# Optimization experiments

Hardware: AMD Instinct MI355X
Metric: run time of the kernel (lower is better)

The kernel has to match this reference:

```python
import jax, jax.numpy as jnp
import numpy as np

B, S, D, H, F = 2, 2048, 1024, 16, 4096
HD = D // H
EPS = 1e-5
NEG = -1e9


def _layernorm(x, g, b):
    mu = jnp.mean(x, axis=-1, keepdims=True)
    var = jnp.mean((x - mu) ** 2, axis=-1, keepdims=True)
    return (x - mu) * jax.lax.rsqrt(var + EPS) * g + b


def _attention(x, wq, wk, wv, wo, bo):
    b, s, d = x.shape
    q = (x @ wq).reshape(b, s, H, HD).transpose(0, 2, 1, 3)  # [b,h,s,hd]
    k = (x @ wk).reshape(b, s, H, HD).transpose(0, 2, 1, 3)
    v = (x @ wv).reshape(b, s, H, HD).transpose(0, 2, 1, 3)
    scores = jnp.einsum('bhqd,bhkd->bhqk', q, k) / (HD ** 0.5)
    # Faithful to source bug: masked_fill(mask == 0, -1e9) where mask = triu(diag=1)
    # -> positions with k <= q (lower triangle incl. diagonal) are filled with -1e9.
    lower = jnp.tril(jnp.ones((s, s), dtype=bool))
    scores = jnp.where(lower, NEG, scores)
    w = jax.nn.softmax(scores, axis=-1)
    o = jnp.einsum('bhqk,bhkd->bhqd', w, v)
    o = o.transpose(0, 2, 1, 3).reshape(b, s, d)
    return o @ wo + bo


def _ffn(x, w1, b1, w2, b2):
    return jax.nn.gelu(x @ w1 + b1, approximate=False) @ w2 + b2


def setup_inputs() -> dict:
    key = jax.random.key(0)
    ks = jax.random.split(key, 10)
    s = 0.02
    return {
        'x': jax.random.normal(ks[0], (B, S, D), jnp.float32),
        'wq': jax.random.normal(ks[1], (D, D), jnp.float32) * s,
        'wk': jax.random.normal(ks[2], (D, D), jnp.float32) * s,
        'wv': jax.random.normal(ks[3], (D, D), jnp.float32) * s,
        'wo': jax.random.normal(ks[4], (D, D), jnp.float32) * s,
        'bo': jnp.zeros((D,), jnp.float32),
        'ln1_g': jnp.ones((D,), jnp.float32),
        'ln1_b': jnp.zeros((D,), jnp.float32),
        'ln2_g': jnp.ones((D,), jnp.float32),
        'ln2_b': jnp.zeros((D,), jnp.float32),
        'w1': jax.random.normal(ks[5], (D, F), jnp.float32) * s,
        'b1': jnp.zeros((F,), jnp.float32),
        'w2': jax.random.normal(ks[6], (F, D), jnp.float32) * s,
        'b2': jnp.zeros((D,), jnp.float32),
    }


def reference(x, wq, wk, wv, wo, bo, ln1_g, ln1_b, ln2_g, ln2_b, w1, b1, w2, b2):
    shortcut = x
    h = _layernorm(x, ln1_g, ln1_b)
    h = _attention(h, wq, wk, wv, wo, bo)  # dropout = identity (eval)
    h = h + shortcut
    shortcut = h
    h2 = _layernorm(h, ln2_g, ln2_b)
    h2 = _attention(h2, wq, wk, wv, wo, bo)  # same attn module reused, per source
    h2 = _ffn(h2, w1, b1, w2, b2)
    return h2 + shortcut
```

## Files before the change

### kernel.cpp

```cpp
#include <hip/hip_runtime.h>
#include <hip/hip_bf16.h>
#include <math.h>

#define Bz 2
#define Sz 2048
#define Dz 1024
#define Hz 16
#define HDz 64
#define Fz 4096
#define ROWS (Bz*Sz)
#define EPSf 1e-5f
#define NEGf -1e9f
#define SC2f 0.1803368801111204f

typedef __attribute__((ext_vector_type(8))) short short8;
typedef __attribute__((ext_vector_type(4))) float floatx4;

__device__ __forceinline__ unsigned short f2bf(float f){
  __hip_bfloat16 h = __float2bfloat16(f);
  return *(unsigned short*)&h;
}
__device__ __forceinline__ float bf2f(unsigned short u){
  union { unsigned x; float f; } a; a.x = ((unsigned)u) << 16; return a.f;
}

__device__ __forceinline__ float fast_gelu(float x){
  float t  = fabsf(x) * 0.70710678118654752f;
  float kk = __builtin_amdgcn_rcpf(1.0f + 0.3275911f * t);
  float poly = ((((1.061405429f*kk - 1.453152027f)*kk + 1.421413741f)*kk
                 - 0.284496736f)*kk + 0.254829592f)*kk;
  float er = 1.0f - poly * __expf(-t*t);
  er = copysignf(er, x);
  return 0.5f * x * (1.0f + er);
}

__device__ __forceinline__ void gload16(const void* g, void* l){
  __builtin_amdgcn_global_load_lds(
      (const __attribute__((address_space(1))) unsigned int*)g,
      (__attribute__((address_space(3))) unsigned int*)l, 16, 0, 0);
}

__device__ __forceinline__ void bar(){
  asm volatile("" ::: "memory");
  __builtin_amdgcn_s_barrier();
  asm volatile("" ::: "memory");
}
#define WAITV6 asm volatile("s_waitcnt vmcnt(6)" ::: "memory")
#define WAITV4 asm volatile("s_waitcnt vmcnt(4)" ::: "memory")
#define WAITV0 asm volatile("s_waitcnt vmcnt(0)" ::: "memory")
#define WL0    asm volatile("s_waitcnt lgkmcnt(0)" ::: "memory")

__device__ __forceinline__ void xcd_remap(int& bmblk, int& bnblk){
  int gx = gridDim.x, gy = gridDim.y;
  int id = blockIdx.y * gx + blockIdx.x;
  int xcd = id & 7, local = id >> 3;
  bnblk = local % gx;
  bmblk = xcd * (gy >> 3) + local / gx;
}

__device__ __forceinline__ void tc_body(const float* __restrict__ W,
                                        unsigned short* __restrict__ Wt,
                                        int K, int N, int n0, int k0)
{
  __shared__ unsigned short Ts[32][33];
  int r = threadIdx.x >> 3, c0 = (threadIdx.x & 7) * 4;
  float4 w4 = *(const float4*)(W + (size_t)(k0+r)*N + n0 + c0);
  Ts[r][c0+0] = f2bf(w4.x); Ts[r][c0+1] = f2bf(w4.y);
  Ts[r][c0+2] = f2bf(w4.z); Ts[r][c0+3] = f2bf(w4.w);
  __syncthreads();
  unsigned v0 = Ts[c0+0][r], v1 = Ts[c0+1][r], v2 = Ts[c0+2][r], v3 = Ts[c0+3][r];
  uint2 p; p.x = v0 | (v1<<16); p.y = v2 | (v3<<16);
  *(uint2*)(Wt + (size_t)(n0+r)*K + k0 + c0) = p;
}

__global__ __launch_bounds__(256)
void transpose_qkvo(const float* __restrict__ w0, unsigned short* __restrict__ t0,
                    const float* __restrict__ w1, unsigned short* __restrict__ t1,
                    const float* __restrict__ w2, unsigned short* __restrict__ t2,
                    const float* __restrict__ w3, unsigned short* __restrict__ t3)
{
  int z = blockIdx.z;
  const float* W = z==0 ? w0 : z==1 ? w1 : z==2 ? w2 : w3;
  unsigned short* T = z==0 ? t0 : z==1 ? t1 : z==2 ? t2 : t3;
  tc_body(W, T, Dz, Dz, blockIdx.x*32, blockIdx.y*32);
}

__global__ __launch_bounds__(256)
void transpose_ffn(const float* __restrict__ w1, unsigned short* __restrict__ w1T,
                   const float* __restrict__ w2, unsigned short* __restrict__ w2T)
{
  int z = blockIdx.z;
  const float* W = z ? w2 : w1;
  unsigned short* T = z ? w2T : w1T;
  int K = z ? Fz : Dz, N = z ? Dz : Fz;
  int n0 = (z ? blockIdx.y : blockIdx.x) * 32;
  int k0 = (z ? blockIdx.x : blockIdx.y) * 32;
  tc_body(W, T, K, N, n0, k0);
}

__global__ __launch_bounds__(256)
void transpose_bf(const unsigned short* __restrict__ V, unsigned short* __restrict__ VT,
                  float* __restrict__ vsum)
{
  __shared__ unsigned short Ts[32][33];
  int st = blockIdx.x*32;
  int R0 = blockIdx.y*32;
  int b = R0 >> 10, hd0 = R0 & 1023;
  int r = threadIdx.x >> 3, c0 = (threadIdx.x & 7) * 4;
  uint2 w = *(const uint2*)(V + (size_t)(b*Sz + st + r)*Dz + hd0 + c0);
  Ts[r][c0+0] = (unsigned short)(w.x & 0xffff);
  Ts[r][c0+1] = (unsigned short)(w.x >> 16);
  Ts[r][c0+2] = (unsigned short)(w.y & 0xffff);
  Ts[r][c0+3] = (unsigned short)(w.y >> 16);
  __syncthreads();
  unsigned v0 = Ts[c0+0][r], v1 = Ts[c0+1][r], v2 = Ts[c0+2][r], v3 = Ts[c0+3][r];
  uint2 p; p.x = v0 | (v1<<16); p.y = v2 | (v3<<16);
  *(uint2*)(VT + (size_t)(R0+r)*Sz + st + c0) = p;
  float s = bf2f((unsigned short)v0) + bf2f((unsigned short)v1)
          + bf2f((unsigned short)v2) + bf2f((unsigned short)v3);
  s += __shfl_down(s, 1, 8);
  s += __shfl_down(s, 2, 8);
  s += __shfl_down(s, 4, 8);
  if ((threadIdx.x & 7) == 0) atomicAdd(vsum + R0 + r, s);
}

__global__ __launch_bounds__(256)
void ln_kernel(const float* __restrict__ in, const float* __restrict__ gam,
               const float* __restrict__ bet, unsigned short* __restrict__ out)
{
  int row = blockIdx.x, t = threadIdx.x;
  size_t base = (size_t)row * Dz;
  int c0 = t * 4;
  float4 x4 = *(const float4*)(in + base + c0);
  float v[4] = {x4.x, x4.y, x4.z, x4.w};
  float s = v[0]+v[1]+v[2]+v[3];
  #pragma unroll
  for (int off=32; off>0; off>>=1) s += __shfl_down(s, off, 64);
  __shared__ float ws[4];
  int lane = t & 63, wid = t >> 6;
  if (lane == 0) ws[wid] = s;
  __syncthreads();
  float mu = (ws[0]+ws[1]+ws[2]+ws[3]) * (1.0f/Dz);
  __syncthreads();
  float d0=v[0]-mu, d1=v[1]-mu, d2=v[2]-mu, d3=v[3]-mu;
  float s2 = d0*d0+d1*d1+d2*d2+d3*d3;
  #pragma unroll
  for (int off=32; off>0; off>>=1) s2 += __shfl_down(s2, off, 64);
  if (lane == 0) ws[wid] = s2;
  __syncthreads();
  float var = (ws[0]+ws[1]+ws[2]+ws[3]) * (1.0f/Dz);
  float rstd = rsqrtf(var + EPSf);
  float4 g4 = *(const float4*)(gam + c0);
  float4 b4 = *(const float4*)(bet + c0);
  unsigned r0 = f2bf((v[0]-mu)*rstd*g4.x + b4.x);
  unsigned r1 = f2bf((v[1]-mu)*rstd*g4.y + b4.y);
  unsigned r2 = f2bf((v[2]-mu)*rstd*g4.z + b4.z);
  unsigned r3 = f2bf((v[3]-mu)*rstd*g4.w + b4.w);
  uint2 p; p.x = r0 | (r1<<16); p.y = r2 | (r3<<16);
  *(uint2*)(out + base + c0) = p;
}

#define STG_A(buf, half, k0) { \
  _Pragma("unroll") for (int c_=0;c_<2;c_++){ \
    int sg_ = c_*8 + wave; \
    int row0_ = ((sg_>>3)<<7) + ((sg_&7)<<3) + ((half)<<6); \
    gload16(pA[half][c_] + (k0), &As[buf][row0_*64]); } }

#define STG_B(buf, jh, k0) { \
  _Pragma("unroll") for (int c_=0;c_<2;c_++){ \
    int sg_ = c_*8 + wave; int rho0_ = sg_<<3; \
    gload16(pB[jh][c_] + (k0), &Bs[buf][jh][rho0_*64]); } }

#define READ_A4(dst, buf, ihalf) { \
  _Pragma("unroll") for (int ii_=0; ii_<4; ++ii_){ \
    int row_ = wm*128 + ((ihalf)*4+ii_)*16 + l15; \
    _Pragma("unroll") for (int ks_=0; ks_<2; ++ks_){ \
      int slot_ = (ks_*4+quad) ^ (l15&7); \
      dst[ii_][ks_] = *(const short8*)&As[buf][row_*64 + slot_*8]; } } }

#define READ_B2(dst, buf, jh) { \
  _Pragma("unroll") for (int jl_=0; jl_<2; ++jl_){ \
    int rho_ = wn*32 + jl_*16 + l15; \
    _Pragma("unroll") for (int ks_=0; ks_<2; ++ks_){ \
      int slot_ = (ks_*4+quad) ^ (l15&7); \
      dst[jl_][ks_] = *(const short8*)&Bs[buf][jh][rho_*64 + slot_*8]; } } }

#define MFMA_PH(IH, JH, AF, BF) { \
  __builtin_amdgcn_s_setprio(1); \
  _Pragma("unroll") for (int ii_=0; ii_<4; ++ii_){ \
    _Pragma("unroll") for (int jl_=0; jl_<2; ++jl_){ \
      floatx4 c_ = acc[(IH)*4+ii_][(JH)*2+jl_]; \
      c_ = __builtin_amdgcn_mfma_f32_16x16x32_bf16(AF[ii_][0], BF[jl_][0], c_, 0,0,0); \
      c_ = __builtin_amdgcn_mfma_f32_16x16x32_bf16(AF[ii_][1], BF[jl_][1], c_, 0,0,0); \
      acc[(IH)*4+ii_][(JH)*2+jl_] = c_; } } \
  __builtin_amdgcn_s_setprio(0); }

template<int SCHED>
__global__ __launch_bounds__(512, 2)
void gemm256(const unsigned short* __restrict__ A,
             const unsigned short* __restrict__ Bt,
             const float* __restrict__ bias, const float* __restrict__ res,
             float* __restrict__ outf, unsigned short* __restrict__ outb,
             int M, int N, int K, int lda, int ldb, int act, int qkvmode)
{
  __shared__ unsigned short As[2][256*64];
  __shared__ unsigned short Bs[2][2][128*64];

  int t = threadIdx.x;
  int wave = t >> 6, lane = t & 63;
  int l15 = lane & 15, quad = lane >> 4;
  int wm = wave >> 2, wn = wave & 3;

  int nN = gridDim.x, nM = gridDim.y;
  int id = blockIdx.y * nN + blockIdx.x;
  int xcd = id & 7, local = id >> 3;
  int bnblk = local % nN;
  int bmblk = xcd * (nM >> 3) + local / nN;
  int bm = bmblk * 256, bn = bnblk * 256;

  if (gridDim.z > 1){
    A    += (size_t)blockIdx.z * K;
    Bt   += (size_t)blockIdx.z * K;
    outf += (size_t)blockIdx.z * ((size_t)M * N);
  }

  int lrow = lane >> 3;
  int lcol = ((lane & 7) ^ (lane >> 3)) * 8;

  const unsigned short* pA[2][2];
  const unsigned short* pB[2][2];
  #pragma unroll
  for (int half=0; half<2; half++)
    #pragma unroll
    for (int c=0;c<2;c++){
      int sg = c*8 + wave;
      int row0 = ((sg>>3)<<7) + ((sg&7)<<3) + (half<<6);
      pA[half][c] = A + (size_t)(bm + row0 + lrow)*lda + lcol;
    }
  #pragma unroll
  for (int jh=0; jh<2; jh++)
    #pragma unroll
    for (int c=0;c<2;c++){
      int sg = c*8 + wave;
      int rho0 = sg<<3;
      int gn = ((rho0>>5)<<6) + (jh<<5) + (rho0&31);
      pB[jh][c] = Bt + (size_t)(bn + gn + lrow)*ldb + lcol;
    }

  floatx4 acc[8][4];
  #pragma unroll
  for (int i=0;i<8;i++)
    #pragma unroll
    for (int j=0;j<4;j++) acc[i][j] = (floatx4){0.f,0.f,0.f,0.f};

  int NKT = K >> 6;
  int nIter = NKT >> 1;

  if constexpr (SCHED == 0) {
    STG_A(0, 0, 0);  STG_A(0, 1, 0);
    STG_B(0, 0, 0);  STG_B(0, 1, 0);
    STG_A(1, 0, 64); STG_A(1, 1, 64);
    STG_B(1, 0, 64);
    WAITV6;
    bar();

    for (int it = 0; it < nIter; ++it){
      bool more = (it + 1 < nIter);
      int k0B  = (2*it+1) << 6;
      int k0A2 = (2*it+2) << 6;
      int k0B2 = (2*it+3) << 6;
      short8 aLo[4][2], aHi[4][2], bcur[2][2];

      READ_A4(aLo, 0, 0);
      READ_B2(bcur, 0, 0);
      STG_B(1, 1, k0B);
      WL0; bar();
      MFMA_PH(0, 0, aLo, bcur);

      READ_A4(aHi, 0, 1);
      if (more) STG_A(0, 0, k0A2);
      WL0; bar();
      MFMA_PH(1, 0, aHi, bcur);

      READ_B2(bcur, 0, 1);
      if (more) STG_A(0, 1, k0A2);
      WL0; bar();
      MFMA_PH(1, 1, aHi, bcur);

      if (more) { STG_B(0, 0, k0A2); WAITV6; }
      else      { WAITV0; }
      bar();
      MFMA_PH(0, 1, aLo, bcur);

      READ_A4(aLo, 1, 0);
      READ_B2(bcur, 1, 0);
      if (more) STG_B(0, 1, k0A2);
      WL0; bar();
      MFMA_PH(0, 0, aLo, bcur);

      READ_A4(aHi, 1, 1);
      if (more) STG_A(1, 0, k0B2);
      WL0; bar();
      MFMA_PH(1, 0, aHi, bcur);

      READ_B2(bcur, 1, 1);
      if (more) STG_A(1, 1, k0B2);
      WL0; bar();
      MFMA_PH(1, 1, aHi, bcur);

      if (more) { STG_B(1, 0, k0B2); WAITV6; }
      bar();
      MFMA_PH(0, 1, aLo, bcur);
    }
  } else {
    STG_A(0, 0, 0);  STG_A(0, 1, 0);
    STG_B(0, 0, 0);  STG_B(0, 1, 0);
    STG_B(1, 0, 64); STG_B(1, 1, 64);
    WAITV4;
    bar();

    for (int it = 0; it < nIter; ++it){
      bool more = (it + 1 < nIter);
      int k0B  = (2*it+1) << 6;
      int k0A2 = (2*it+2) << 6;
      int k0B2 = (2*it+3) << 6;
      short8 aLo[4][2], aHi[4][2], b01[2][2], b23[2][2];

      READ_A4(aLo, 0, 0);
      READ_B2(b01, 0, 0);
      READ_B2(b23, 0, 1);
      STG_A(1, 0, k0B); STG_A(1, 1, k0B);
      WL0; bar();
      MFMA_PH(0, 0, aLo, b01);
      MFMA_PH(0, 1, aLo, b23);

      READ_A4(aHi, 0, 1);
      if (more) { STG_A(0, 0, k0A2); STG_B(0, 0, k0A2); WAITV4; }
      else      { WAITV0; }
      WL0; bar();
      MFMA_PH(1, 0, aHi, b01);
      MFMA_PH(1, 1, aHi, b23);

      READ_A4(aLo, 1, 0);
      READ_B2(b01, 1, 0);
      READ_B2(b23, 1, 1);
      if (more) { STG_A(0, 1, k0A2); STG_B(0, 1, k0A2); }
      WL0; bar();
      MFMA_PH(0, 0, aLo, b01);
      MFMA_PH(0, 1, aLo, b23);

      READ_A4(aHi, 1, 1);
      if (more) { STG_B(1, 0, k0B2); STG_B(1, 1, k0B2); WAITV4; }
      WL0; bar();
      MFMA_PH(1, 0, aHi, b01);
      MFMA_PH(1, 1, aHi, b23);
    }
  }

  float bj[4];
  #pragma unroll
  for (int j=0;j<4;j++) bj[j] = bias ? bias[bn + wn*64 + j*16 + l15] : 0.f;

  size_t selbase = 0; int ncol = N; int bnl = bn;
  if (qkvmode){ selbase = (size_t)(bn >> 10) * ((size_t)M * 1024); ncol = 1024; bnl = bn & 1023; }

  #pragma unroll
  for (int i=0;i<8;i++){
    int row0 = bm + wm*128 + i*16 + quad*4;
    #pragma unroll
    for (int r=0;r<4;r++){
      size_t rowoff = selbase + (size_t)(row0 + r) * ncol;
      #pragma unroll
      for (int j=0;j<4;j++){
        float v = acc[i][j][r] + bj[j];
        if (act) v = fast_gelu(v);
        size_t off = rowoff + bnl + wn*64 + j*16 + l15;
        if (res) v += res[off];
        if (outf) outf[off] = v;
        else      outb[off] = f2bf(v);
      }
    }
  }
}

__global__ __launch_bounds__(256)
void gemm_n64(const unsigned short* __restrict__ A,
              const unsigned short* __restrict__ Bt,
              const float* __restrict__ bias, const float* __restrict__ res,
              float* __restrict__ outf, unsigned short* __restrict__ outb,
              int M, int N, int K)
{
  __shared__ unsigned short As[2][128*64];
  __shared__ unsigned short Bs[2][64*64];
  int t = threadIdx.x;
  int bmblk, bnblk; xcd_remap(bmblk, bnblk);
  int bm = bmblk * 128, bn = bnblk * 64;
  int wave = t >> 6, lane = t & 63;
  int l15 = lane & 15, quad = lane >> 4;
  int swr = l15 & 7;
  int arow = lane >> 3;
  int acbg = ((lane & 7) ^ arow) * 8;
  const unsigned short* gA = A  + (size_t)(bm + wave*32 + arow)*K + acbg;
  const unsigned short* gB = Bt + (size_t)(bn + wave*16 + arow)*K + acbg;

  floatx4 acc[2][4];
  #pragma unroll
  for (int i=0;i<2;i++)
    #pragma unroll
    for (int j=0;j<4;j++) acc[i][j] = (floatx4){0.f,0.f,0.f,0.f};

  {
    unsigned short* lA = &As[0][wave*32*64];
    unsigned short* lB = &Bs[0][wave*16*64];
    gload16(gA,                 lA);
    gload16(gA + (size_t)8*K,   lA + 8*64);
    gload16(gA + (size_t)16*K,  lA + 16*64);
    gload16(gA + (size_t)24*K,  lA + 24*64);
    gload16(gB,                 lB);
    gload16(gB + (size_t)8*K,   lB + 8*64);
  }

  int nIter = K >> 6;
  for (int it = 0; it < nIter; ++it) {
    __syncthreads();
    int cur = it & 1;
    if (it + 1 < nIter) {
      int k1 = (it+1) << 6;
      unsigned short* lA = &As[cur^1][wave*32*64];
      unsigned short* lB = &Bs[cur^1][wave*16*64];
      gload16(gA + k1,                 lA);
      gload16(gA + k1 + (size_t)8*K,   lA + 8*64);
      gload16(gA + k1 + (size_t)16*K,  lA + 16*64);
      gload16(gA + k1 + (size_t)24*K,  lA + 24*64);
      gload16(gB + k1,                 lB);
      gload16(gB + k1 + (size_t)8*K,   lB + 8*64);
    }
    const unsigned short* Ac = As[cur];
    const unsigned short* Bc = Bs[cur];
    #pragma unroll
    for (int ks=0; ks<2; ++ks){
      short8 af[2], bf[4];
      #pragma unroll
      for (int i=0;i<2;i++)
        af[i] = *(const short8*)&Ac[(wave*32 + i*16 + l15)*64 + ((ks*4 + quad) ^ swr)*8];
      #pragma unroll
      for (int j=0;j<4;j++)
        bf[j] = *(const short8*)&Bc[(j*16 + l15)*64 + ((ks*4 + quad) ^ swr)*8];
      #pragma unroll
      for (int i=0;i<2;i++)
        #pragma unroll
        for (int j=0;j<4;j++)
          acc[i][j] = __builtin_amdgcn_mfma_f32_16x16x32_bf16(af[i], bf[j], acc[i][j], 0, 0, 0);
    }
  }

  float bj[4];
  #pragma unroll
  for (int j=0;j<4;j++) bj[j] = bias ? bias[bn + j*16 + l15] : 0.f;

  #pragma unroll
  for (int i=0;i<2;i++){
    int row0 = bm + wave*32 + i*16 + quad*4;
    #pragma unroll
    for (int r=0;r<4;r++){
      size_t rowoff = (size_t)(row0 + r) * N;
      #pragma unroll
      for (int j=0;j<4;j++){
        float v = acc[i][j][r] + bj[j];
        size_t off = rowoff + bn + j*16 + l15;
        if (res) v += res[off];
        if (outf) outf[off] = v;
        else      outb[off] = f2bf(v);
      }
    }
  }
}

__global__ __launch_bounds__(256)
void reduce4(const float* __restrict__ part, const float* __restrict__ bias,
             const float* __restrict__ res, float* __restrict__ out)
{
  const size_t NN = (size_t)ROWS * Dz;
  size_t i = ((size_t)blockIdx.x * 256 + threadIdx.x) * 4;
  float4 a = *(const float4*)(part + i);
  float4 b = *(const float4*)(part + NN + i);
  float4 c = *(const float4*)(part + 2*NN + i);
  float4 d = *(const float4*)(part + 3*NN + i);
  float4 r = *(const float4*)(res + i);
  int col = threadIdx.x * 4;
  float4 g = *(const float4*)(bias + col);
  float4 o;
  o.x = a.x+b.x+c.x+d.x + g.x + r.x;
  o.y = a.y+b.y+c.y+d.y + g.y + r.y;
  o.z = a.z+b.z+c.z+d.z + g.z + r.z;
  o.w = a.w+b.w+c.w+d.w + g.w + r.w;
  *(float4*)(out + i) = o;
}

#define ATT_STAGE_KV() { \
    *(uint4*)&Ks[sr*64 + ((kc2  ) ^ ksw)*8] = pk0; \
    *(uint4*)&Ks[sr*64 + ((kc2+1) ^ ksw)*8] = pk1; \
    *(uint4*)&Vts[vd*128 + (((vk8  )&8) | (((vk8  )^vsw)&7))*8] = pv0; \
    *(uint4*)&Vts[vd*128 + (((vk8+1)&8) | (((vk8+1)^vsw)&7))*8] = pv1; }

#define ATT_PREFETCH(tile) { \
    size_t off0_ = ((size_t)(b*Sz + (tile)*128 + sr))*Dz + h*HDz + sc; \
    pk0 = *(const uint4*)(Kg + off0_); pk1 = *(const uint4*)(Kg + off0_ + 8); \
    int vo_ = (tile)*128 + vc*16; \
    pv0 = *(const uint4*)(vrow + vo_); pv1 = *(const uint4*)(vrow + vo_ + 8); }

#define ATT_COMPUTE(MASKED) { \
  _Pragma("unroll") \
  for (int hh=0; hh<2; ++hh){ \
    floatx4 acc_s[4]; \
    _Pragma("unroll") for (int j=0;j<4;j++) acc_s[j] = (floatx4){0.f,0.f,0.f,0.f}; \
    __builtin_amdgcn_s_setprio(1); \
    _Pragma("unroll") \
    for (int ks=0;ks<2;ks++){ \
      short8 bk[4]; \
      _Pragma("unroll") \
      for (int j=0;j<4;j++) \
        bk[j] = *(const short8*)&Ks[(hh*64 + j*16 + l15)*64 + (((ks*4+quad) ^ (l15&7)))*8]; \
      _Pragma("unroll") \
      for (int j=0;j<4;j++) \
        acc_s[j] = __builtin_amdgcn_mfma_f32_16x16x32_bf16(aq[ks], bk[j], acc_s[j], 0, 0, 0); \
    } \
    __builtin_amdgcn_s_setprio(0); \
    _Pragma("unroll") \
    for (int j=0;j<4;j++){ \
      _Pragma("unroll") \
      for (int r=0;r<4;r++){ \
        float s2 = acc_s[j][r] * SC2f; \
        if (MASKED){ int kloc = hh*64 + j*16 + l15; if (kloc <= qloc + r) s2 = NEGf; } \
        float p = __builtin_amdgcn_exp2f(fminf(s2, 115.41f)); \
        lacc[r] += p; \
        Ps[wave*16 + quad*4 + r][j*16 + l15] = f2bf(p); \
      } \
    } \
    __builtin_amdgcn_s_setprio(1); \
    _Pragma("unroll") \
    for (int ks=0;ks<2;ks++){ \
      short8 ap, bv[4]; \
      ap = *(const short8*)&Ps[wave*16 + l15][ks*32 + quad*8]; \
      _Pragma("unroll") \
      for (int j=0;j<4;j++) \
        bv[j] = *(const short8*)&Vts[(j*16 + l15)*128 + (hh*8 + ((ks*4+quad) ^ (l15&7)))*8]; \
      _Pragma("unroll") \
      for (int j=0;j<4;j++) \
        acc_o[j] = __builtin_amdgcn_mfma_f32_16x16x32_bf16(ap, bv[j], acc_o[j], 0, 0, 0); \
    } \
    __builtin_amdgcn_s_setprio(0); \
  } }

__global__ __launch_bounds__(512, 4)
void attn_mfma(const unsigned short* __restrict__ Qg,
               const unsigned short* __restrict__ Kg,
               const unsigned short* __restrict__ VTg,
               const float* __restrict__ vmean,
               unsigned short* __restrict__ Og)
{
  __shared__ unsigned short Ks[128*64];
  __shared__ unsigned short Vts[64*128];
  __shared__ unsigned short Ps[128][72];

  int t = threadIdx.x;
  int wave = t >> 6, lane = t & 63;
  int l15 = lane & 15, quad = lane >> 4;
  int b = blockIdx.z, h = blockIdx.y;
  int qt = b ? (15 - (int)blockIdx.x) : (int)blockIdx.x;

  {
    int r = t >> 2, c = (t & 3) * 16;
    const unsigned short* qp = Qg + ((size_t)(b*Sz + qt*128 + r))*Dz + h*HDz + c;
    uint4 q0 = *(const uint4*)(qp);
    uint4 q1 = *(const uint4*)(qp + 8);
    *(uint4*)&Ps[r][c]     = q0;
    *(uint4*)&Ps[r][c + 8] = q1;
  }

  int sr = t >> 2, sc = (t & 3) * 16;
  int kc2 = (t & 3) * 2, ksw = sr & 7;
  int vd = t >> 3, vc = t & 7, vsw = vd & 7;
  int vk8 = vc * 2;
  const unsigned short* vrow = VTg + ((size_t)((b*Hz + h)*64 + vd))*Sz;

  uint4 pk0, pk1, pv0, pv1;
  ATT_PREFETCH(qt);

  __syncthreads();
  short8 aq[2];
  aq[0] = *(const short8*)&Ps[wave*16 + l15][quad*8];
  aq[1] = *(const short8*)&Ps[wave*16 + l15][32 + quad*8];

  floatx4 acc_o[4];
  #pragma unroll
  for (int j=0;j<4;j++) acc_o[j] = (floatx4){0.f,0.f,0.f,0.f};
  float lacc[4] = {0.f, 0.f, 0.f, 0.f};

  int qloc = wave*16 + quad*4;

  ATT_STAGE_KV();
  __syncthreads();
  if (qt + 1 < Sz/128) ATT_PREFETCH(qt+1);
  ATT_COMPUTE(1);

  for (int jt2 = qt+1; jt2 < Sz/128; ++jt2){
    __syncthreads();
    ATT_STAGE_KV();
    __syncthreads();
    if (jt2 + 1 < Sz/128) ATT_PREFETCH(jt2+1);
    ATT_COMPUTE(0);
  }

  #pragma unroll
  for (int r=0;r<4;r++){
    float l = lacc[r];
    l += __shfl_xor(l, 1, 64);
    l += __shfl_xor(l, 2, 64);
    l += __shfl_xor(l, 4, 64);
    l += __shfl_xor(l, 8, 64);
    int qrow = qt*128 + wave*16 + quad*4 + r;
    float inv = 1.0f / l;
    size_t rowoff = ((size_t)(b*Sz + qrow))*Dz + h*HDz;
    #pragma unroll
    for (int j=0;j<4;j++){
      float ov = acc_o[j][r] * inv;
      if (qrow == Sz-1) ov = vmean[(b*Hz + h)*HDz + j*16 + l15] * (1.0f/2048.0f);
      Og[rowoff + j*16 + l15] = f2bf(ov);
    }
  }
}

extern "C" void kernel_launch(void* const* d_in, const int* in_sizes, int n_in,
                              void* d_out, int out_size, void* d_ws, size_t ws_size,
                              hipStream_t stream)
{
  const float* x    = (const float*)d_in[0];
  const float* wq   = (const float*)d_in[1];
  const float* wk   = (const float*)d_in[2];
  const float* wv   = (const float*)d_in[3];
  const float* wo   = (const float*)d_in[4];
  const float* bo   = (const float*)d_in[5];
  const float* ln1g = (const float*)d_in[6];
  const float* ln1b = (const float*)d_in[7];
  const float* ln2g = (const float*)d_in[8];
  const float* ln2b = (const float*)d_in[9];
  const float* w1   = (const float*)d_in[10];
  const float* b1   = (const float*)d_in[11];
  const float* w2   = (const float*)d_in[12];
  const float* b2   = (const float*)d_in[13];
  float* out = (float*)d_out;

  const size_t MB = 1024*1024;
  char* w = (char*)d_ws;
  float*          trunk = (float*)(w);
  unsigned short* lnb   = (unsigned short*)(w + 16*MB);
  unsigned short* q     = (unsigned short*)(w + 24*MB);
  unsigned short* k     = (unsigned short*)(w + 32*MB);
  unsigned short* v     = (unsigned short*)(w + 40*MB);
  unsigned short* ctx   = (unsigned short*)(w + 48*MB);
  unsigned short* wqkvT = (unsigned short*)(w + 56*MB);
  unsigned short* wqT   = wqkvT;
  unsigned short* wkT   = (unsigned short*)(w + 58*MB);
  unsigned short* wvT   = (unsigned short*)(w + 60*MB);
  unsigned short* woT   = (unsigned short*)(w + 62*MB);
  unsigned short* w1T   = (unsigned short*)(w + 64*MB);
  unsigned short* w2T   = (unsigned short*)(w + 72*MB);
  unsigned short* mid   = (unsigned short*)(w + 24*MB);
  float*          part  = (float*)(w + 80*MB);
  bool splitk = ws_size >= (size_t)144*MB;

  unsigned short* vT    = (unsigned short*)d_out;
  float*          vmean = (float*)((char*)d_out + 8*MB);

  dim3 blk(256), blk512(512);
  transpose_qkvo<<<dim3(32,32,4), blk, 0, stream>>>(wq, wqT, wk, wkT, wv, wvT, wo, woT);
  transpose_ffn<<<dim3(128,32,2), blk, 0, stream>>>(w1, w1T, w2, w2T);

  dim3 gln(ROWS);
  dim3 gqkv(3*Dz/256, ROWS/256);
  dim3 gf1(Fz/256,  ROWS/256);
  dim3 gn64(Dz/64,  ROWS/128);
  dim3 gattn(Sz/128, Hz, Bz);
  dim3 gvt(Sz/32, Bz*Hz*HDz/32);

  ln_kernel<<<gln, blk, 0, stream>>>(x, ln1g, ln1b, lnb);
  gemm256<0><<<gqkv, blk512, 0, stream>>>(lnb, wqkvT, nullptr, nullptr, nullptr, q, ROWS, 3*Dz, Dz, Dz, Dz, 0, 1);
  hipMemsetAsync(vmean, 0, 2048*sizeof(float), stream);
  transpose_bf<<<gvt, blk, 0, stream>>>(v, vT, vmean);
  attn_mfma<<<gattn, blk512, 0, stream>>>(q, k, vT, vmean, ctx);
  gemm_n64<<<gn64, blk, 0, stream>>>(ctx, woT, bo, x, trunk, nullptr, ROWS, Dz, Dz);

  ln_kernel<<<gln, blk, 0, stream>>>(trunk, ln2g, ln2b, lnb);
  gemm256<0><<<gqkv, blk512, 0, stream>>>(lnb, wqkvT, nullptr, nullptr, nullptr, q, ROWS, 3*Dz, Dz, Dz, Dz, 0, 1);
  hipMemsetAsync(vmean, 0, 2048*sizeof(float), stream);
  transpose_bf<<<gvt, blk, 0, stream>>>(v, vT, vmean);
  attn_mfma<<<gattn, blk512, 0, stream>>>(q, k, vT, vmean, ctx);
  gemm_n64<<<gn64, blk, 0, stream>>>(ctx, woT, bo, nullptr, nullptr, lnb, ROWS, Dz, Dz);
  gemm256<1><<<gf1, blk512, 0, stream>>>(lnb, w1T, b1, nullptr, nullptr, mid, ROWS, Fz, Dz, Dz, Dz, 1, 0);
  if (splitk) {
    gemm256<1><<<dim3(4,16,4), blk512, 0, stream>>>(mid, w2T, nullptr, nullptr, part, nullptr, ROWS, Dz, Fz/4, Fz, Fz, 0, 0);
    reduce4<<<dim3(4096), blk, 0, stream>>>(part, b2, trunk, out);
  } else {
    gemm_n64<<<gn64, blk, 0, stream>>>(mid, w2T, b2, trunk, out, nullptr, ROWS, Dz, Fz);
  }
}
```

Baseline: 452.0 us.

## Triple-buffer gemm_n64 LDS pipeline with prefetch depth two and explicit waits

Converts the N=64 GEMM kernel from double to triple buffering in shared memory. It prefetches two K-tiles ahead, reads all LDS fragments before issuing the next global-to-LDS loads, then uses explicit vmcnt/lgkmcnt waits and a single barrier before the MFMAs. The goal is to hide global load latency better and drop one barrier per iteration. In exchange the kernel uses more shared memory, which may reduce occupancy, and needs more registers to hold both k-substeps of fragments.

```diff
diff --git a/kernel.cpp b/kernel.cpp
--- a/kernel.cpp
+++ b/kernel.cpp
@@ -383,6 +383,16 @@
   }
 }
 
+#define N64_STG(buf, k0) { \
+    unsigned short* lA_ = &As[buf][wave*32*64]; \
+    unsigned short* lB_ = &Bs[buf][wave*16*64]; \
+    gload16(gA + (k0),                 lA_); \
+    gload16(gA + (k0) + (size_t)8*K,   lA_ + 8*64); \
+    gload16(gA + (k0) + (size_t)16*K,  lA_ + 16*64); \
+    gload16(gA + (k0) + (size_t)24*K,  lA_ + 24*64); \
+    gload16(gB + (k0),                 lB_); \
+    gload16(gB + (k0) + (size_t)8*K,   lB_ + 8*64); }
+
 __global__ __launch_bounds__(256)
 void gemm_n64(const unsigned short* __restrict__ A,
               const unsigned short* __restrict__ Bt,
@@ -390,8 +400,8 @@
               float* __restrict__ outf, unsigned short* __restrict__ outb,
               int M, int N, int K)
 {
-  __shared__ unsigned short As[2][128*64];
-  __shared__ unsigned short Bs[2][64*64];
+  __shared__ unsigned short As[3][128*64];
+  __shared__ unsigned short Bs[3][64*64];
   int t = threadIdx.x;
   int bmblk, bnblk; xcd_remap(bmblk, bnblk);
   int bm = bmblk * 128, bn = bnblk * 64;
@@ -409,49 +419,42 @@
     #pragma unroll
     for (int j=0;j<4;j++) acc[i][j] = (floatx4){0.f,0.f,0.f,0.f};
 
-  {
-    unsigned short* lA = &As[0][wave*32*64];
-    unsigned short* lB = &Bs[0][wave*16*64];
-    gload16(gA,                 lA);
-    gload16(gA + (size_t)8*K,   lA + 8*64);
-    gload16(gA + (size_t)16*K,  lA + 16*64);
-    gload16(gA + (size_t)24*K,  lA + 24*64);
-    gload16(gB,                 lB);
-    gload16(gB + (size_t)8*K,   lB + 8*64);
-  }
+  N64_STG(0, 0);
+  N64_STG(1, 64);
+  WAITV6;
+  bar();
 
   int nIter = K >> 6;
+  int cur = 0;
   for (int it = 0; it < nIter; ++it) {
-    __syncthreads();
-    int cur = it & 1;
-    if (it + 1 < nIter) {
-      int k1 = (it+1) << 6;
-      unsigned short* lA = &As[cur^1][wave*32*64];
-      unsigned short* lB = &Bs[cur^1][wave*16*64];
-      gload16(gA + k1,                 lA);
-      gload16(gA + k1 + (size_t)8*K,   lA + 8*64);
-      gload16(gA + k1 + (size_t)16*K,  lA + 16*64);
-      gload16(gA + k1 + (size_t)24*K,  lA + 24*64);
-      gload16(gB + k1,                 lB);
-      gload16(gB + k1 + (size_t)8*K,   lB + 8*64);
-    }
     const unsigned short* Ac = As[cur];
     const unsigned short* Bc = Bs[cur];
+    short8 af[2][2], bf[2][4];
     #pragma unroll
     for (int ks=0; ks<2; ++ks){
-      short8 af[2], bf[4];
       #pragma unroll
       for (int i=0;i<2;i++)
-        af[i] = *(const short8*)&Ac[(wave*32 + i*16 + l15)*64 + ((ks*4 + quad) ^ swr)*8];
+        af[ks][i] = *(const short8*)&Ac[(wave*32 + i*16 + l15)*64 + ((ks*4 + quad) ^ swr)*8];
       #pragma unroll
       for (int j=0;j<4;j++)
-        bf[j] = *(const short8*)&Bc[(j*16 + l15)*64 + ((ks*4 + quad) ^ swr)*8];
+        bf[ks][j] = *(const short8*)&Bc[(j*16 + l15)*64 + ((ks*4 + quad) ^ swr)*8];
+    }
+    if (it + 2 < nIter) {
+      int nb = cur + 2; if (nb >= 3) nb -= 3;
+      N64_STG(nb, (it+2) << 6);
+    }
+    WL0;
+    if (it + 2 < nIter)      { WAITV6; }
+    else if (it + 1 < nIter) { WAITV0; }
+    bar();
+    #pragma unroll
+    for (int ks=0; ks<2; ++ks)
       #pragma unroll
       for (int i=0;i<2;i++)
         #pragma unroll
         for (int j=0;j<4;j++)
-          acc[i][j] = __builtin_amdgcn_mfma_f32_16x16x32_bf16(af[i], bf[j], acc[i][j], 0, 0, 0);
-    }
+          acc[i][j] = __builtin_amdgcn_mfma_f32_16x16x32_bf16(af[ks][i], bf[ks][j], acc[i][j], 0, 0, 0);
+    cur = (cur == 2) ? 0 : cur + 1;
   }
 
   float bj[4];
```

New measurement: 573.2 us. +26.8%, slower.
